# Optimization experiments

Hardware: AMD Instinct MI355X
Metric: run time of the kernel (lower is better)

## Reference

```python
import jax, jax.numpy as jnp
import numpy as np

STRIDES = (8.0, 16.0, 32.0)
SCORE_T = 0.25
NMS_T = 0.45
DET = 100          # max detections per image
PRE_NMS = 1000     # static top-k surrogate for torch.where score filtering
MAX_SIZE = 4096.0  # class offset for batched (class-aware) NMS
IMG = 640.0        # image side (square), used for box clamping
ANCHORS = np.array([[[10,13],[16,30],[33,23]],
                    [[30,61],[62,45],[59,119]],
                    [[116,90],[156,198],[373,326]]], dtype=np.float32)


def setup_inputs() -> dict:
    key = jax.random.key(0)
    k0, k1, k2 = jax.random.split(key, 3)
    return {
        "pred0": jax.random.normal(k0, (16, 80, 80, 3, 85), dtype=jnp.float32),
        "pred1": jax.random.normal(k1, (16, 40, 40, 3, 85), dtype=jnp.float32),
        "pred2": jax.random.normal(k2, (16, 20, 20, 3, 85), dtype=jnp.float32),
        "anchors": jnp.asarray(ANCHORS),
        "scale_factors": jnp.ones((16,), dtype=jnp.float32),
    }


def _decode_level(pred, stride, anc):
    # pred: [B,H,W,A,5+C], anc: [A,2]
    p = jax.nn.sigmoid(pred)
    B, H, W, A, E = p.shape
    C = E - 5
    gx, gy = jnp.meshgrid(jnp.arange(W, dtype=p.dtype),
                          jnp.arange(H, dtype=p.dtype), indexing='xy')
    grid = jnp.stack((gx, gy), -1)                      # [H,W,2] = (x,y)
    xy = (2.0 * p[..., :2] - 0.5 + grid[None, :, :, None, :]) * stride
    wh = 4.0 * jnp.square(p[..., 2:4]) * anc            # [B,H,W,A,2]
    boxes = jnp.concatenate((xy - wh * 0.5, xy + wh * 0.5), -1)  # cxcywh->xyxy
    obj = p[..., 4:5]
    s = obj * p[..., 5:]                                # [B,H,W,A,C]
    s = jnp.where((obj > SCORE_T) & (s > SCORE_T), s, 0.0)
    return boxes.reshape(B, -1, 4), s.reshape(B, -1, C)


def _box_iou_1n(box, boxes):
    # box [4], boxes [K,4] -> iou [K]
    lt = jnp.maximum(box[:2], boxes[:, :2])
    rb = jnp.minimum(box[2:], boxes[:, 2:])
    wh = jnp.clip(rb - lt, 0.0)
    inter = wh[:, 0] * wh[:, 1]
    a1 = (box[2] - box[0]) * (box[3] - box[1])
    a2 = (boxes[:, 2] - boxes[:, 0]) * (boxes[:, 3] - boxes[:, 1])
    return inter / (a1 + a2 - inter + 1e-7)


def _per_image(boxes, scores, scale):
    # boxes [M,4], scores [M,C]
    C = scores.shape[-1]
    topv, topi = jax.lax.top_k(scores.reshape(-1), PRE_NMS)
    bidx = topi // C
    lab = topi % C
    bx = boxes[bidx]                                    # [K,4]
    obx = bx + lab.astype(bx.dtype)[:, None] * MAX_SIZE  # class-offset boxes

    def body(i, st):
        sc, keep, ks = st
        j = jnp.argmax(sc)
        keep = keep.at[i].set(j)
        ks = ks.at[i].set(sc[j])
        iou = _box_iou_1n(obx[j], obx)
        sc = jnp.where(iou > NMS_T, 0.0, sc)
        return sc, keep, ks

    st0 = (topv, jnp.zeros((DET,), jnp.int32), jnp.zeros((DET,), bx.dtype))
    _, keep, ks = jax.lax.fori_loop(0, DET, body, st0)
    kb = bx[keep] / scale
    kl = lab[keep].astype(bx.dtype)
    valid = ks > 0
    kb = jnp.where(valid[:, None], kb, 0.0)
    kl = jnp.where(valid, kl, -1.0)
    return jnp.concatenate((kb, ks[:, None], kl[:, None]), -1)  # [DET,6]


def reference(pred0, pred1, pred2, anchors, scale_factors):
    preds = (pred0, pred1, pred2)
    bs, ss = [], []
    for lvl, (pred, stride) in enumerate(zip(preds, STRIDES)):
        b, s = _decode_level(pred, stride, anchors[lvl])
        bs.append(b)
        ss.append(s)
    boxes = jnp.clip(jnp.concatenate(bs, 1), 0.0, IMG)   # [B,M,4]
    scores = jnp.concatenate(ss, 1)                      # [B,M,C]
    return jax.vmap(_per_image)(boxes, scores, scale_factors)  # [B,DET,6]
```

## Files before the change

### kernel.cpp

```cpp
#include <hip/hip_runtime.h>
#include <cstdint>
#include <cstddef>

#pragma clang fp contract(off)

constexpr int NIMG  = 16;
constexpr int NB0   = 19200;
constexpr int NB1   = 4800;
constexpr int NB2   = 1200;
constexpr int NBOX  = 25200;
constexpr int NCLS  = 80;
constexpr int NCH   = 85;
constexpr int NBINS = 4096;
constexpr int CAP   = 4096;
constexpr int NTOP  = 1000;
constexpr int NDET  = 100;
constexpr float IMGSZ = 640.0f;
constexpr float BIN_SCALE = 4096.0f / 0.75f;

constexpr int TILE    = 128;
constexpr int TILES   = (NBOX + TILE - 1) / TILE;

constexpr int IOU_RPB = 40;
constexpr int LOWBIN  = 2048;
constexpr int NFINE   = NBINS - LOWBIN;
constexpr float LUMP_S = 0.25f + (float)LOWBIN / BIN_SCALE;

typedef float float4a __attribute__((ext_vector_type(4), aligned(4)));
typedef float float2a __attribute__((ext_vector_type(2), aligned(4)));

__device__ __forceinline__ float xla_expf(float x) {
  const float kLog2e = 1.44269504088896341f;
  const float kC1 = 0.693359375f;
  const float kC2 = -2.12194440e-4f;
  const float cp0 = 1.9875691500e-4f;
  const float cp1 = 1.3981999507e-3f;
  const float cp2 = 8.3334519073e-3f;
  const float cp3 = 4.1665795894e-2f;
  const float cp4 = 1.6666665459e-1f;
  const float cp5 = 5.0000001201e-1f;
  float xc = fminf(x, 88.3762626647950f);
  xc = fmaxf(xc, -88.3762626647949f);
  float fx = floorf(fmaf(xc, kLog2e, 0.5f));
  float xr = fmaf(fx, -kC1, xc);
  xr = fmaf(fx, -kC2, xr);
  float z = xr * xr;
  float y = fmaf(cp0, xr, cp1);
  y = fmaf(y, xr, cp2);
  y = fmaf(y, xr, cp3);
  y = fmaf(y, xr, cp4);
  y = fmaf(y, xr, cp5);
  y = fmaf(y, z, xr);
  y = y + 1.0f;
  int n = (int)fx;
  float two_n = __int_as_float((n + 127) << 23);
  float r = y * two_n;
  return fmaxf(r, xc);
}

__device__ __forceinline__ float ref_sigmoid(float x) {
  return 1.0f / (1.0f + xla_expf(-x));
}

__device__ __forceinline__ float fast_sigmoid(float x) {
  float e = __expf(-x);
  return __fdividef(1.0f, 1.0f + e);
}

__device__ __forceinline__ int score_bin(float s) {
  int b = (int)((s - 0.25f) * BIN_SCALE);
  return min(max(b, 0), NBINS - 1);
}

__device__ __forceinline__ const float* locate(int img, int box,
    const float* __restrict__ p0, const float* __restrict__ p1, const float* __restrict__ p2,
    int& lvl, int& gx, int& gy, int& anc, float& stride) {
  const float* base; int r, W;
  if (box < NB0)            { lvl = 0; r = box;             W = 80; base = p0 + (size_t)img * NB0 * NCH; stride = 8.0f;  }
  else if (box < NB0 + NB1) { lvl = 1; r = box - NB0;       W = 40; base = p1 + (size_t)img * NB1 * NCH; stride = 16.0f; }
  else                      { lvl = 2; r = box - NB0 - NB1; W = 20; base = p2 + (size_t)img * NB2 * NCH; stride = 32.0f; }
  anc = r % 3;
  int cell = r / 3;
  gx = cell % W;
  gy = cell / W;
  return base + (size_t)r * NCH;
}

__device__ __forceinline__ float clip640(float v) {
  return fminf(fmaxf(v, 0.0f), IMGSZ);
}

__device__ __forceinline__ const float* row_ptr(int img, int box,
    const float* __restrict__ p0, const float* __restrict__ p1, const float* __restrict__ p2) {
  const float* base; int r;
  if (box < NB0)            { base = p0 + (size_t)img * NB0 * NCH; r = box; }
  else if (box < NB0 + NB1) { base = p1 + (size_t)img * NB1 * NCH; r = box - NB0; }
  else                      { base = p2 + (size_t)img * NB2 * NCH; r = box - NB0 - NB1; }
  return base + (size_t)r * NCH;
}

__global__ __launch_bounds__(256) void k_passA(const float* __restrict__ p0,
    const float* __restrict__ p1, const float* __restrict__ p2,
    unsigned int* __restrict__ ghist, unsigned short* __restrict__ maxbin) {
  __shared__ unsigned int histF[NFINE];
  const int tid = threadIdx.x;
  const int img  = blockIdx.x / TILES;
  const int tile = blockIdx.x % TILES;
  const int tbase = tile * TILE;
  const int nbox_tile = min(TILE, NBOX - tbase);
  const int lane = tid & 63;

  for (int i = tid; i < NFINE; i += 256) histF[i] = 0u;
  __syncthreads();

  const int b_local = tid >> 3, part = tid & 7;
  int lowc = 0;

  float   xoR[4];
  float4a vaR[4], vbR[4];
  float2a vcR[4];

  #pragma unroll
  for (int s = 0; s < TILE / 32; ++s) {
    int bl_ = s * 32 + b_local;
    int box_ = tbase + min(bl_, nbox_tile - 1);
    const float* row_ = row_ptr(img, box_, p0, p1, p2);
    xoR[s] = row_[4];
    const float* cls_ = row_ + 5 + 10 * part;
    vaR[s] = *(const float4a*)(cls_);
    vbR[s] = *(const float4a*)(cls_ + 4);
    vcR[s] = *(const float2a*)(cls_ + 8);
  }

  #pragma unroll
  for (int step = 0; step < TILE / 32; ++step) {
    int bl = step * 32 + b_local;
    bool valid = (bl < nbox_tile);
    float xo = xoR[step];
    float v[10] = { vaR[step].x, vaR[step].y, vaR[step].z, vaR[step].w,
                    vbR[step].x, vbR[step].y, vbR[step].z, vbR[step].w,
                    vcR[step].x, vcR[step].y };

    float obj = 0.0f, tcons = 3.0e38f, thi = 3.0e38f;
    if (part == 0) {
      obj = fast_sigmoid(xo);
      if (valid && obj > 0.2499f) {
        float rr = 0.2499f / obj;
        tcons = __logf(__fdividef(rr, 1.0f - rr)) - 0.05f;
        float rh = LUMP_S / obj;
        if (rh < 1.0f) thi = __logf(__fdividef(rh, 1.0f - rh)) - 0.05f;
      }
    }
    obj   = __shfl(obj,   0, 8);
    tcons = __shfl(tcons, 0, 8);
    thi   = __shfl(thi,   0, 8);

    int mb = 0;
    #pragma unroll
    for (int k = 0; k < 10; ++k) {
      float x = v[k];
      if (x > tcons) {
        if (x > thi) {
          float s = obj * fast_sigmoid(x);
          if (s > 0.2499f) {
            int bin = score_bin(s);
            if (bin >= LOWBIN) {
              atomicAdd(&histF[bin - LOWBIN], 1u);
              mb = max(mb, bin + 1);
            } else {
              ++lowc;
              mb = max(mb, bin + 1);
            }
          }
        } else {
          ++lowc;
          mb = max(mb, LOWBIN);
        }
      }
    }
    mb = max(mb, __shfl_xor(mb, 1, 8));
    mb = max(mb, __shfl_xor(mb, 2, 8));
    mb = max(mb, __shfl_xor(mb, 4, 8));
    if (valid && part == 0)
      maxbin[(size_t)img * NBOX + tbase + bl] = (unsigned short)mb;
  }

  #pragma unroll
  for (int d = 1; d < 64; d <<= 1) lowc += __shfl_xor(lowc, d);
  if (lane == 0 && lowc) atomicAdd(&ghist[img * NBINS + 0], (unsigned int)lowc);
  __syncthreads();

  for (int i = tid; i < NFINE; i += 256) {
    unsigned int v2 = histF[i];
    if (v2) atomicAdd(&ghist[img * NBINS + LOWBIN + i], v2);
  }
}

__global__ __launch_bounds__(256) void k_thresh(const unsigned int* __restrict__ ghist,
                                                int* __restrict__ tbin) {
  __shared__ unsigned int h[NBINS];
  __shared__ unsigned int psum[256];
  const int tid = threadIdx.x;
  const int img = blockIdx.x;

  for (int i = tid; i < NBINS; i += 256) h[i] = ghist[img * NBINS + i];
  __syncthreads();
  unsigned int ps = 0;
  for (int k = 0; k < 16; ++k) ps += h[tid * 16 + k];
  psum[tid] = ps;
  __syncthreads();
  if (tid == 0) {
    long long cum = 0;
    int tb = 0;
    bool found = false;
    for (int g = 255; g >= 0 && !found; --g) {
      if (cum + (long long)psum[g] >= NTOP) {
        for (int b = g * 16 + 15; b >= g * 16; --b) {
          cum += h[b];
          if (cum >= NTOP) { tb = b; found = true; break; }
        }
      } else {
        cum += psum[g];
      }
    }
    if (!found) tb = 0;
    int tc = (tb >= 2) ? tb - 2 : 0;
    for (int b = tb - 1; b >= tc; --b) cum += h[b];
    while (cum > CAP - 8 && tc < NBINS - 1) { cum -= h[tc]; ++tc; }
    tbin[img] = tc;
  }
}

__global__ __launch_bounds__(256) void k_wlemit(const float* __restrict__ p0,
    const float* __restrict__ p1, const float* __restrict__ p2,
    const unsigned short* __restrict__ maxbin, const int* __restrict__ tbin,
    unsigned long long* __restrict__ cand, int* __restrict__ cnt) {
  __shared__ unsigned int list[256];
  __shared__ int lcnt;
  const int tid = threadIdx.x;
  const int lane = tid & 63;
  if (tid == 0) lcnt = 0;
  __syncthreads();

  int idx = blockIdx.x * 256 + tid;
  if (idx < NIMG * NBOX) {
    int img = idx / NBOX;
    int box = idx - img * NBOX;
    if ((int)maxbin[idx] > tbin[img])
      list[atomicAdd(&lcnt, 1)] = ((unsigned int)img << 16) | (unsigned int)box;
  }
  __syncthreads();
  const int n = lcnt;
  const int nsweep = (n + 31) / 32;

  for (int s = 0; s < nsweep; ++s) {
    int r = s * 32 + (tid >> 3);
    int part = tid & 7;
    bool have = (r < n);
    int img = 0, box = 0, nc = 0;
    unsigned int bm = 0;
    float obj_e = -1.0f;
    float v[10];
    if (have) {
      unsigned int e = list[r];
      img = (int)(e >> 16);
      box = (int)(e & 0xFFFFu);
      const float* row = row_ptr(img, box, p0, p1, p2);
      float xo = row[4];
      float obj_f = fast_sigmoid(xo);
      if (obj_f > 0.2499f) {
        const float* cls = row + 5 + 10 * part;
        float4a va = *(const float4a*)(cls);
        float4a vb = *(const float4a*)(cls + 4);
        float2a vc = *(const float2a*)(cls + 8);
        v[0]=va.x; v[1]=va.y; v[2]=va.z; v[3]=va.w;
        v[4]=vb.x; v[5]=vb.y; v[6]=vb.z; v[7]=vb.w;
        v[8]=vc.x; v[9]=vc.y;
        int tc = tbin[img];
        #pragma unroll
        for (int k = 0; k < 10; ++k) {
          float sf = obj_f * fast_sigmoid(v[k]);
          if (sf > 0.2499f && score_bin(sf) >= tc) {
            if (obj_e < 0.0f) obj_e = ref_sigmoid(xo);
            if (obj_e > 0.25f) {
              float se = obj_e * ref_sigmoid(v[k]);
              if (se > 0.25f) { bm |= 1u << k; ++nc; }
            }
          }
        }
      }
    }

    int mybase = 0;
    unsigned long long active = __ballot(nc > 0);
    while (active) {
      int leader = __ffsll(active) - 1;
      int limg = __shfl(img, leader);
      bool mine = (nc > 0) && (img == limg);
      unsigned long long grp = __ballot(mine);
      int incl = mine ? nc : 0;
      #pragma unroll
      for (int d = 1; d < 64; d <<= 1) {
        int t = __shfl_up(incl, d);
        if (lane >= d) incl += t;
      }
      int hi = 63 - __clzll(grp);
      int total = __shfl(incl, hi);
      int base = 0;
      if (lane == leader) base = atomicAdd(&cnt[limg], total);
      base = __shfl(base, leader);
      if (mine) mybase = base + incl - nc;
      active &= ~grp;
    }

    if (nc > 0) {
      int pos = mybase;
      #pragma unroll
      for (int k = 0; k < 10; ++k) {
        if (bm & (1u << k)) {
          float se = obj_e * ref_sigmoid(v[k]);
          if (pos < CAP) {
            unsigned int fi = (unsigned int)(box * NCLS + 10 * part + k);
            unsigned long long key =
                ((unsigned long long)__float_as_uint(se) << 32) |
                (unsigned long long)(0xFFFFFFFFu - fi);
            cand[(size_t)img * CAP + pos] = key;
          }
          ++pos;
        }
      }
    }
  }
}

#define SIDX(i) ((i) + ((i) >> 4))

__global__ __launch_bounds__(1024) void k_sort(const float* __restrict__ p0,
    const float* __restrict__ p1, const float* __restrict__ p2,
    const float* __restrict__ anchors, const unsigned long long* __restrict__ cand,
    const int* __restrict__ cnt_arr, float* __restrict__ boxes8) {
  __shared__ unsigned long long keys[CAP + CAP / 16];
  __shared__ int n2_sh, cnt_sh;
  const int tid = threadIdx.x;
  const int img = blockIdx.x;

  if (tid == 0) {
    int c = cnt_arr[img];
    c = max(0, min(c, CAP));
    int n2 = 1024;
    while (n2 < c) n2 <<= 1;
    cnt_sh = c; n2_sh = n2;
  }
  __syncthreads();
  const int cnt = cnt_sh;
  const int n2  = n2_sh;

  const unsigned long long* c = cand + (size_t)img * CAP;
  for (int i = tid; i < n2; i += 1024) keys[SIDX(i)] = (i < cnt) ? c[i] : 0ull;
  __syncthreads();

  for (int kk = 2; kk <= n2; kk <<= 1) {
    for (int j = kk >> 1; j > 0; j >>= 1) {
      for (int i = tid; i < n2; i += 1024) {
        int l = i ^ j;
        if (l > i) {
          unsigned long long a = keys[SIDX(i)], b = keys[SIDX(l)];
          bool up = ((i & kk) == 0);
          bool sw = up ? (a < b) : (a > b);
          if (sw) { keys[SIDX(i)] = b; keys[SIDX(l)] = a; }
        }
      }
      __syncthreads();
    }
  }

  float* dst = boxes8 + (size_t)img * NTOP * 8;
  if (tid < NTOP) {
    int i = tid;
    unsigned long long key = keys[SIDX(i)];
    unsigned int v = (unsigned int)(key >> 32);
    float4 fa, fb;
    if (v) {
      unsigned int idx = 0xFFFFFFFFu - (unsigned int)(key & 0xFFFFFFFFu);
      int box = (int)(idx / NCLS);
      int l   = (int)(idx % NCLS);
      int lvl, gx, gy, anc; float stride;
      const float* ptr = locate(img, box, p0, p1, p2, lvl, gx, gy, anc, stride);
      float sx = ref_sigmoid(ptr[0]);
      float sy = ref_sigmoid(ptr[1]);
      float sw = ref_sigmoid(ptr[2]);
      float sh = ref_sigmoid(ptr[3]);
      float aw = anchors[(lvl * 3 + anc) * 2 + 0];
      float ah = anchors[(lvl * 3 + anc) * 2 + 1];
      float cx = (2.0f * sx - 0.5f + (float)gx) * stride;
      float cy = (2.0f * sy - 0.5f + (float)gy) * stride;
      float ww = (4.0f * (sw * sw)) * aw;
      float hh = (4.0f * (sh * sh)) * ah;
      fa.x = clip640(cx - ww * 0.5f);
      fa.y = clip640(cy - hh * 0.5f);
      fa.z = clip640(cx + ww * 0.5f);
      fa.w = clip640(cy + hh * 0.5f);
      fb.x = __uint_as_float(v);
      fb.y = (float)l;
      fb.z = 0.0f; fb.w = 0.0f;
    } else {
      fa.x = fa.y = fa.z = fa.w = 0.0f;
      fb.x = 0.0f; fb.y = -1.0f; fb.z = 0.0f; fb.w = 0.0f;
    }
    *(float4*)(dst + i * 8)     = fa;
    *(float4*)(dst + i * 8 + 4) = fb;
  }
}

__global__ __launch_bounds__(256) void k_iou(const float* __restrict__ boxes8,
                                             unsigned int* __restrict__ mat) {
  __shared__ float obx[NTOP * 5];
  const int img = blockIdx.x / (NTOP / IOU_RPB);
  const int rg  = blockIdx.x % (NTOP / IOU_RPB);
  const float* src = boxes8 + (size_t)img * NTOP * 8;

  for (int t = threadIdx.x; t < NTOP; t += 256) {
    float4 fa = *(const float4*)(src + t * 8);
    float lab = src[t * 8 + 5];
    float off = lab * 4096.0f;
    obx[t * 5 + 0] = fa.x + off;
    obx[t * 5 + 1] = fa.y + off;
    obx[t * 5 + 2] = fa.z + off;
    obx[t * 5 + 3] = fa.w + off;
  }
  __syncthreads();

  const int wave = threadIdx.x >> 6;
  const int lane = threadIdx.x & 63;
  for (int task = wave; task < IOU_RPB * 16; task += 4) {
    int r = rg * IOU_RPB + (task >> 4);
    int w = task & 15;
    float a0 = obx[r * 5 + 0], a1 = obx[r * 5 + 1];
    float a2 = obx[r * 5 + 2], a3 = obx[r * 5 + 3];
    float areaA = (a2 - a0) * (a3 - a1);
    int col = w * 64 + lane;
    bool bit = false;
    if (col < NTOP) {
      float o0 = obx[col * 5 + 0], o1 = obx[col * 5 + 1];
      float o2 = obx[col * 5 + 2], o3 = obx[col * 5 + 3];
      float ltx = fmaxf(a0, o0);
      float lty = fmaxf(a1, o1);
      float rbx = fminf(a2, o2);
      float rby = fminf(a3, o3);
      float wx = fmaxf(rbx - ltx, 0.0f);
      float wy = fmaxf(rby - lty, 0.0f);
      float inter = wx * wy;
      float a2r = (o2 - o0) * (o3 - o1);
      float denom = areaA + a2r - inter + 1e-7f;
      bit = (inter / denom) > 0.45f;
    }
    unsigned long long m = __ballot(bit);
    if (lane == 0)
      *(unsigned long long*)(mat + ((size_t)img * NTOP + r) * 32 + w * 2) = m;
  }
}

__global__ __launch_bounds__(256) void k_nms(const unsigned int* __restrict__ mat,
    const float* __restrict__ boxes8, const float* __restrict__ scalef,
    float* __restrict__ out) {
  __shared__ uint4 mat_lds4[NTOP * 8];
  unsigned int* mat_lds = (unsigned int*)mat_lds4;
  const int tid = threadIdx.x;
  const int lane = tid & 63;
  const int img = blockIdx.x;
  const float* src = boxes8 + (size_t)img * NTOP * 8;

  const uint4* msrc = (const uint4*)(mat + (size_t)img * NTOP * 32);
  for (int i = tid; i < NTOP * 8; i += 256) mat_lds4[i] = msrc[i];
  __syncthreads();
  if (tid >= 64) return;

  unsigned int aw = 0u;
  for (int w = 0; w < 16; ++w) {
    int t = w * 64 + lane;
    float va = (t < NTOP) ? src[t * 8 + 4] : 0.0f;
    unsigned long long b = __ballot(va > 0.0f);
    if (lane == 2 * w)     aw = (unsigned int)b;
    if (lane == 2 * w + 1) aw = (unsigned int)(b >> 32);
  }
  if (lane >= 32) aw = 0u;

  int pj0 = -1, pj1 = -1;
  for (int i = 0; i < NDET; ++i) {
    unsigned long long bal = __ballot(aw != 0u);
    int j = -1;
    if (bal != 0ull) {
      int L = __ffsll(bal) - 1;
      unsigned int wL = (unsigned int)__shfl((int)aw, L);
      j = L * 32 + (__ffs(wL) - 1);
    }
    if (lane == (i & 63)) { if (i < 64) pj0 = j; else pj1 = j; }
    if (j >= 0 && lane < 32) aw &= ~mat_lds[j * 32 + lane];
  }

  const float scf = scalef[img];
  #pragma unroll
  for (int rep = 0; rep < 2; ++rep) {
    int i = rep * 64 + lane;
    if (i >= NDET) break;
    int j = (rep == 0) ? pj0 : pj1;
    float* orow = out + ((size_t)img * NDET + i) * 6;
    if (j < 0) {
      orow[0] = 0.0f; orow[1] = 0.0f; orow[2] = 0.0f;
      orow[3] = 0.0f; orow[4] = 0.0f; orow[5] = -1.0f;
    } else {
      float4 fa = *(const float4*)(src + j * 8);
      float va = src[j * 8 + 4];
      float lb = src[j * 8 + 5];
      orow[0] = fa.x / scf; orow[1] = fa.y / scf;
      orow[2] = fa.z / scf; orow[3] = fa.w / scf;
      orow[4] = va;
      orow[5] = lb;
    }
  }
}

extern "C" void kernel_launch(void* const* d_in, const int* in_sizes, int n_in,
                              void* d_out, int out_size, void* d_ws, size_t ws_size,
                              hipStream_t stream) {
  const float* p0 = (const float*)d_in[0];
  const float* p1 = (const float*)d_in[1];
  const float* p2 = (const float*)d_in[2];
  const float* anchors = (const float*)d_in[3];
  const float* scalef  = (const float*)d_in[4];
  float* out = (float*)d_out;

  char* w = (char*)d_ws;
  unsigned int* ghist = (unsigned int*)(w);
  int* cnt  = (int*)(w + 262144);
  int* tbin = (int*)(w + 262208);
  unsigned long long* cand = (unsigned long long*)(w + 262336);
  unsigned short* maxbin = (unsigned short*)(w + 262336 + 524288);
  float* boxes8 = (float*)(w + 786624 + 806400 + 64);
  unsigned int* mat = (unsigned int*)(w + 1593088 + 512000);

  hipMemsetAsync(ghist, 0, 262144 + 192, stream);

  k_passA<<<dim3(NIMG * TILES), dim3(256), 0, stream>>>(p0, p1, p2, ghist, maxbin);
  k_thresh<<<dim3(NIMG), dim3(256), 0, stream>>>(ghist, tbin);
  k_wlemit<<<dim3((NIMG * NBOX + 255) / 256), dim3(256), 0, stream>>>(p0, p1, p2, maxbin, tbin, cand, cnt);
  k_sort<<<dim3(NIMG), dim3(1024), 0, stream>>>(p0, p1, p2, anchors, cand, cnt, boxes8);
  k_iou<<<dim3(NIMG * (NTOP / IOU_RPB)), dim3(256), 0, stream>>>(boxes8, mat);
  k_nms<<<dim3(NIMG), dim3(256), 0, stream>>>(mat, boxes8, scalef, out);
}
```

Before: 182.5 us.

## Fuse threshold scan into emit kernel and IoU matrix into NMS kernel

Removes the separate k_thresh kernel: every emit block now reloads its image's histogram and recomputes the threshold bin locally. Emit blocks are re-tiled per image, so the per-image segmented wave scan reduces to one plain scan. The IoU bitmask kernel is merged into NMS: one 1024-thread block per image builds the 1000x1000 mask in LDS and then runs the greedy pass, which removes two launches and the global mask round trip. In exchange, the histogram work is repeated in every emit block, and the IoU matrix now runs on only 16 blocks instead of 400, so that stage has much less parallelism.

```diff
diff --git a/kernel.cpp b/kernel.cpp
--- a/kernel.cpp
+++ b/kernel.cpp
@@ -21,10 +21,10 @@
 constexpr int TILE    = 128;
 constexpr int TILES   = (NBOX + TILE - 1) / TILE;
 
-constexpr int IOU_RPB = 40;
 constexpr int LOWBIN  = 2048;
 constexpr int NFINE   = NBINS - LOWBIN;
 constexpr float LUMP_S = 0.25f + (float)LOWBIN / BIN_SCALE;
+constexpr int BPI     = (NBOX + 255) / 256;
 
 typedef float float4a __attribute__((ext_vector_type(4), aligned(4)));
 typedef float float2a __attribute__((ext_vector_type(2), aligned(4)));
@@ -99,6 +99,28 @@
   return base + (size_t)r * NCH;
 }
 
+__device__ __forceinline__ int thresh_scan(const unsigned int* h,
+                                           const unsigned int* psum) {
+  long long cum = 0;
+  int tb = 0;
+  bool found = false;
+  for (int g = 255; g >= 0 && !found; --g) {
+    if (cum + (long long)psum[g] >= NTOP) {
+      for (int b = g * 16 + 15; b >= g * 16; --b) {
+        cum += h[b];
+        if (cum >= NTOP) { tb = b; found = true; break; }
+      }
+    } else {
+      cum += psum[g];
+    }
+  }
+  if (!found) tb = 0;
+  int tc = (tb >= 2) ? tb - 2 : 0;
+  for (int b = tb - 1; b >= tc; --b) cum += h[b];
+  while (cum > CAP - 8 && tc < NBINS - 1) { cum -= h[tc]; ++tc; }
+  return tc;
+}
+
 __global__ __launch_bounds__(256) void k_passA(const float* __restrict__ p0,
     const float* __restrict__ p1, const float* __restrict__ p2,
     unsigned int* __restrict__ ghist, unsigned short* __restrict__ maxbin) {
@@ -196,59 +218,35 @@
   }
 }
 
-__global__ __launch_bounds__(256) void k_thresh(const unsigned int* __restrict__ ghist,
-                                                int* __restrict__ tbin) {
+__global__ __launch_bounds__(256) void k_wlemit(const float* __restrict__ p0,
+    const float* __restrict__ p1, const float* __restrict__ p2,
+    const unsigned int* __restrict__ ghist, const unsigned short* __restrict__ maxbin,
+    unsigned long long* __restrict__ cand, int* __restrict__ cnt) {
   __shared__ unsigned int h[NBINS];
   __shared__ unsigned int psum[256];
-  const int tid = threadIdx.x;
-  const int img = blockIdx.x;
-
-  for (int i = tid; i < NBINS; i += 256) h[i] = ghist[img * NBINS + i];
-  __syncthreads();
-  unsigned int ps = 0;
-  for (int k = 0; k < 16; ++k) ps += h[tid * 16 + k];
-  psum[tid] = ps;
-  __syncthreads();
-  if (tid == 0) {
-    long long cum = 0;
-    int tb = 0;
-    bool found = false;
-    for (int g = 255; g >= 0 && !found; --g) {
-      if (cum + (long long)psum[g] >= NTOP) {
-        for (int b = g * 16 + 15; b >= g * 16; --b) {
-          cum += h[b];
-          if (cum >= NTOP) { tb = b; found = true; break; }
-        }
-      } else {
-        cum += psum[g];
-      }
-    }
-    if (!found) tb = 0;
-    int tc = (tb >= 2) ? tb - 2 : 0;
-    for (int b = tb - 1; b >= tc; --b) cum += h[b];
-    while (cum > CAP - 8 && tc < NBINS - 1) { cum -= h[tc]; ++tc; }
-    tbin[img] = tc;
-  }
-}
-
-__global__ __launch_bounds__(256) void k_wlemit(const float* __restrict__ p0,
-    const float* __restrict__ p1, const float* __restrict__ p2,
-    const unsigned short* __restrict__ maxbin, const int* __restrict__ tbin,
-    unsigned long long* __restrict__ cand, int* __restrict__ cnt) {
   __shared__ unsigned int list[256];
-  __shared__ int lcnt;
+  __shared__ int lcnt, tc_sh;
   const int tid = threadIdx.x;
   const int lane = tid & 63;
+  const int img  = blockIdx.x / BPI;
+  const int tile = blockIdx.x % BPI;
+
+  for (int i = tid; i < NBINS; i += 256) h[i] = ghist[img * NBINS + i];
   if (tid == 0) lcnt = 0;
   __syncthreads();
-
-  int idx = blockIdx.x * 256 + tid;
-  if (idx < NIMG * NBOX) {
-    int img = idx / NBOX;
-    int box = idx - img * NBOX;
-    if ((int)maxbin[idx] > tbin[img])
-      list[atomicAdd(&lcnt, 1)] = ((unsigned int)img << 16) | (unsigned int)box;
-  }
+  {
+    unsigned int ps = 0;
+    for (int k = 0; k < 16; ++k) ps += h[tid * 16 + k];
+    psum[tid] = ps;
+  }
+  __syncthreads();
+  if (tid == 0) tc_sh = thresh_scan(h, psum);
+  __syncthreads();
+  const int tc = tc_sh;
+
+  int box0 = tile * 256 + tid;
+  if (box0 < NBOX && (int)maxbin[(size_t)img * NBOX + box0] > tc)
+    list[atomicAdd(&lcnt, 1)] = (unsigned int)box0;
   __syncthreads();
   const int n = lcnt;
   const int nsweep = (n + 31) / 32;
@@ -257,14 +255,12 @@
     int r = s * 32 + (tid >> 3);
     int part = tid & 7;
     bool have = (r < n);
-    int img = 0, box = 0, nc = 0;
+    int box = 0, nc = 0;
     unsigned int bm = 0;
     float obj_e = -1.0f;
     float v[10];
     if (have) {
-      unsigned int e = list[r];
-      img = (int)(e >> 16);
-      box = (int)(e & 0xFFFFu);
+      box = (int)list[r];
       const float* row = row_ptr(img, box, p0, p1, p2);
       float xo = row[4];
       float obj_f = fast_sigmoid(xo);
@@ -276,7 +272,6 @@
         v[0]=va.x; v[1]=va.y; v[2]=va.z; v[3]=va.w;
         v[4]=vb.x; v[5]=vb.y; v[6]=vb.z; v[7]=vb.w;
         v[8]=vc.x; v[9]=vc.y;
-        int tc = tbin[img];
         #pragma unroll
         for (int k = 0; k < 10; ++k) {
           float sf = obj_f * fast_sigmoid(v[k]);
@@ -291,27 +286,17 @@
       }
     }
 
-    int mybase = 0;
-    unsigned long long active = __ballot(nc > 0);
-    while (active) {
-      int leader = __ffsll(active) - 1;
-      int limg = __shfl(img, leader);
-      bool mine = (nc > 0) && (img == limg);
-      unsigned long long grp = __ballot(mine);
-      int incl = mine ? nc : 0;
-      #pragma unroll
-      for (int d = 1; d < 64; d <<= 1) {
-        int t = __shfl_up(incl, d);
-        if (lane >= d) incl += t;
-      }
-      int hi = 63 - __clzll(grp);
-      int total = __shfl(incl, hi);
-      int base = 0;
-      if (lane == leader) base = atomicAdd(&cnt[limg], total);
-      base = __shfl(base, leader);
-      if (mine) mybase = base + incl - nc;
-      active &= ~grp;
-    }
+    int incl = nc;
+    #pragma unroll
+    for (int d = 1; d < 64; d <<= 1) {
+      int t = __shfl_up(incl, d);
+      if (lane >= d) incl += t;
+    }
+    int total = __shfl(incl, 63);
+    int base = 0;
+    if (lane == 0 && total > 0) base = atomicAdd(&cnt[img], total);
+    base = __shfl(base, 0);
+    int mybase = base + incl - nc;
 
     if (nc > 0) {
       int pos = mybase;
@@ -412,14 +397,18 @@
   }
 }
 
-__global__ __launch_bounds__(256) void k_iou(const float* __restrict__ boxes8,
-                                             unsigned int* __restrict__ mat) {
+__global__ __launch_bounds__(1024) void k_nms(const float* __restrict__ boxes8,
+    const float* __restrict__ scalef, float* __restrict__ out) {
+  __shared__ unsigned long long mat64[NTOP * 16];
   __shared__ float obx[NTOP * 5];
-  const int img = blockIdx.x / (NTOP / IOU_RPB);
-  const int rg  = blockIdx.x % (NTOP / IOU_RPB);
+  unsigned int* mat32 = (unsigned int*)mat64;
+  const int tid = threadIdx.x;
+  const int lane = tid & 63;
+  const int wave = tid >> 6;
+  const int img = blockIdx.x;
   const float* src = boxes8 + (size_t)img * NTOP * 8;
 
-  for (int t = threadIdx.x; t < NTOP; t += 256) {
+  for (int t = tid; t < NTOP; t += 1024) {
     float4 fa = *(const float4*)(src + t * 8);
     float lab = src[t * 8 + 5];
     float off = lab * 4096.0f;
@@ -430,10 +419,8 @@
   }
   __syncthreads();
 
-  const int wave = threadIdx.x >> 6;
-  const int lane = threadIdx.x & 63;
-  for (int task = wave; task < IOU_RPB * 16; task += 4) {
-    int r = rg * IOU_RPB + (task >> 4);
+  for (int task = wave; task < NTOP * 16; task += 16) {
+    int r = task >> 4;
     int w = task & 15;
     float a0 = obx[r * 5 + 0], a1 = obx[r * 5 + 1];
     float a2 = obx[r * 5 + 2], a3 = obx[r * 5 + 3];
@@ -455,23 +442,8 @@
       bit = (inter / denom) > 0.45f;
     }
     unsigned long long m = __ballot(bit);
-    if (lane == 0)
-      *(unsigned long long*)(mat + ((size_t)img * NTOP + r) * 32 + w * 2) = m;
-  }
-}
-
-__global__ __launch_bounds__(256) void k_nms(const unsigned int* __restrict__ mat,
-    const float* __restrict__ boxes8, const float* __restrict__ scalef,
-    float* __restrict__ out) {
-  __shared__ uint4 mat_lds4[NTOP * 8];
-  unsigned int* mat_lds = (unsigned int*)mat_lds4;
-  const int tid = threadIdx.x;
-  const int lane = tid & 63;
-  const int img = blockIdx.x;
-  const float* src = boxes8 + (size_t)img * NTOP * 8;
-
-  const uint4* msrc = (const uint4*)(mat + (size_t)img * NTOP * 32);
-  for (int i = tid; i < NTOP * 8; i += 256) mat_lds4[i] = msrc[i];
+    if (lane == 0) mat64[r * 16 + w] = m;
+  }
   __syncthreads();
   if (tid >= 64) return;
 
@@ -495,7 +467,7 @@
       j = L * 32 + (__ffs(wL) - 1);
     }
     if (lane == (i & 63)) { if (i < 64) pj0 = j; else pj1 = j; }
-    if (j >= 0 && lane < 32) aw &= ~mat_lds[j * 32 + lane];
+    if (j >= 0 && lane < 32) aw &= ~mat32[j * 32 + lane];
   }
 
   const float scf = scalef[img];
@@ -533,18 +505,14 @@
   char* w = (char*)d_ws;
   unsigned int* ghist = (unsigned int*)(w);
   int* cnt  = (int*)(w + 262144);
-  int* tbin = (int*)(w + 262208);
-  unsigned long long* cand = (unsigned long long*)(w + 262336);
-  unsigned short* maxbin = (unsigned short*)(w + 262336 + 524288);
-  float* boxes8 = (float*)(w + 786624 + 806400 + 64);
-  unsigned int* mat = (unsigned int*)(w + 1593088 + 512000);
-
-  hipMemsetAsync(ghist, 0, 262144 + 192, stream);
+  unsigned long long* cand = (unsigned long long*)(w + 262272);
+  unsigned short* maxbin = (unsigned short*)(w + 262272 + 524288);
+  float* boxes8 = (float*)(w + 786560 + 806400 + 64);
+
+  hipMemsetAsync(ghist, 0, 262144 + 64, stream);
 
   k_passA<<<dim3(NIMG * TILES), dim3(256), 0, stream>>>(p0, p1, p2, ghist, maxbin);
-  k_thresh<<<dim3(NIMG), dim3(256), 0, stream>>>(ghist, tbin);
-  k_wlemit<<<dim3((NIMG * NBOX + 255) / 256), dim3(256), 0, stream>>>(p0, p1, p2, maxbin, tbin, cand, cnt);
+  k_wlemit<<<dim3(NIMG * BPI), dim3(256), 0, stream>>>(p0, p1, p2, ghist, maxbin, cand, cnt);
   k_sort<<<dim3(NIMG), dim3(1024), 0, stream>>>(p0, p1, p2, anchors, cand, cnt, boxes8);
-  k_iou<<<dim3(NIMG * (NTOP / IOU_RPB)), dim3(256), 0, stream>>>(boxes8, mat);
-  k_nms<<<dim3(NIMG), dim3(256), 0, stream>>>(mat, boxes8, scalef, out);
-}
+  k_nms<<<dim3(NIMG), dim3(1024), 0, stream>>>(boxes8, scalef, out);
+}
```

New measurement: 428.8 us. 2.35x slower.
